# Performance work log

Measured on AMD Instinct MI355X. Metric: run time of the kernel, lower is better.

## Reference

```python
import jax, jax.numpy as jnp
import numpy as np

N = 50000        # num_nodes
E = 800000       # num_edges
D = 128          # hidden_dim == attention_dim
H = 4            # heads
DK = D // H      # d_k per head
STEP = 0.25      # args.step_size
NSTEPS = 4       # euler steps for t: 0 -> 1


def setup_inputs() -> dict:
    key = jax.random.key(0)
    k0, k1, k2, k3 = jax.random.split(key, 4)
    x = jax.random.normal(k0, (N, D), dtype=jnp.float32)
    edge_index = jax.random.randint(k1, (2, E), 0, N, dtype=jnp.int64)
    W_Q = jax.random.normal(k2, (D, D), dtype=jnp.float32) * 0.02
    b_Q = jnp.zeros((D,), jnp.float32)
    W_K = jax.random.normal(k3, (D, D), dtype=jnp.float32) * 0.02
    b_K = jnp.zeros((D,), jnp.float32)
    return {"x": x, "W_Q": W_Q, "b_Q": b_Q, "W_K": W_K, "b_K": b_K,
            "edge_index": edge_index}


def _segment_softmax(scores, seg, num_segments):
    # numerically-stable softmax over edges grouped by seg (dst node)
    m = jax.ops.segment_max(scores, seg, num_segments=num_segments)
    e = jnp.exp(scores - m[seg])
    s = jax.ops.segment_sum(e, seg, num_segments=num_segments)
    return e / (s[seg] + 1e-16)


def reference(x, W_Q, b_Q, W_K, b_K, edge_index):
    src, dst = edge_index[0], edge_index[1]
    # multi-head Q/K projections: [N, H, DK]
    q = (x @ W_Q + b_Q).reshape(N, H, DK)
    k = (x @ W_K + b_K).reshape(N, H, DK)
    # per-edge scaled-dot scores: [E, H]
    scores = jnp.sum(q[src] * k[dst], axis=-1) / np.sqrt(DK).astype(np.float32)
    # edge softmax normalized over edge[attention_norm_idx]=edge[1] (dst)
    att = _segment_softmax(scores, dst, N)          # [E, H]
    att_mean = jnp.mean(att, axis=1)                # [E] head-averaged, as in GRAND odefunc

    # fixed-step Euler integration of dx/dt = A x - x with A = attention spmm
    def euler_step(state, _):
        ax = jax.ops.segment_sum(att_mean[:, None] * state[dst], src,
                                 num_segments=N)    # ax[src] += att * x[dst]
        return state + STEP * (ax - state), None

    z, _ = jax.lax.scan(euler_step, x, None, length=NSTEPS)
    return z
```

## Files before the change

kernel.cpp:

```cpp
#include <hip/hip_runtime.h>
#include <hip/hip_fp16.h>

#define NODES 50000
#define EDGES 800000
#define HID   128
#define HEADS 4
#define SCORE_SCALE 0.17677669529663687f

#define NBUCK ((NODES + 255) >> 8)
#define CHUNK 4096

typedef unsigned int       u32;
typedef unsigned short     u16;
typedef unsigned long long u64;

typedef __attribute__((ext_vector_type(8))) short bf16x8;
typedef __attribute__((ext_vector_type(4))) float f32x4;

__device__ __forceinline__ u16 f2bf(float f) {
    u32 u = __builtin_bit_cast(u32, f);
    return (u16)((u + 0x7FFFu + ((u >> 16) & 1u)) >> 16);
}
__device__ __forceinline__ float bflo(u32 u) { return __builtin_bit_cast(float, u << 16); }
__device__ __forceinline__ float bfhi(u32 u) { return __builtin_bit_cast(float, u & 0xFFFF0000u); }
__device__ __forceinline__ float bdot2(u32 a, u32 b) {
    return bflo(a) * bflo(b) + bfhi(a) * bfhi(b);
}
__device__ __forceinline__ float2 h2f2(u32 u) {
    __half2 h = __builtin_bit_cast(__half2, u);
    return __half22float2(h);
}
__device__ __forceinline__ u32 f2h2(float a, float b) {
    __half2 h = __floats2half2_rn(a, b);
    return __builtin_bit_cast(u32, h);
}

__global__ __launch_bounds__(256) void wprep(
    const float* __restrict__ Wq, const float* __restrict__ Wk,
    u16* __restrict__ Wqt, u16* __restrict__ Wkt)
{
    int e   = blockIdx.x * 256 + threadIdx.x;
    int mat = e >> 14;
    int idx = e & 16383;
    int k  = idx >> 7;
    int nn = idx & 127;
    const float* W = mat ? Wk : Wq;
    u16*        Wt = mat ? Wkt : Wqt;
    Wt[nn * 128 + k] = f2bf(W[idx]);
}

__global__ __launch_bounds__(256) void gemm_qk_mfma(
    const float* __restrict__ x,
    const u16* __restrict__ Wqt, const float* __restrict__ bq,
    const u16* __restrict__ Wkt, const float* __restrict__ bk,
    u16* __restrict__ qb, u16* __restrict__ kb, u16* __restrict__ xh, int n)
{
    const int l  = threadIdx.x & 63;
    const int w  = threadIdx.x >> 6;
    const int lr = l & 15;
    const int kg = l >> 4;

    const int arow   = blockIdx.x * 64 + w * 16 + lr;
    const bool av    = (arow < n);
    const int  arowc = av ? arow : (n - 1);

    bf16x8 afrag[4];
    #pragma unroll
    for (int ks = 0; ks < 4; ++ks) {
        const float* px = x + (size_t)arowc * HID + ks * 32 + kg * 8;
        float4 p0 = *(const float4*)px;
        float4 p1 = *(const float4*)(px + 4);
        uint4 pk;
        pk.x = (u32)f2bf(p0.x) | ((u32)f2bf(p0.y) << 16);
        pk.y = (u32)f2bf(p0.z) | ((u32)f2bf(p0.w) << 16);
        pk.z = (u32)f2bf(p1.x) | ((u32)f2bf(p1.y) << 16);
        pk.w = (u32)f2bf(p1.z) | ((u32)f2bf(p1.w) << 16);
        afrag[ks] = __builtin_bit_cast(bf16x8, pk);
        if (av) {
            uint4 ph;
            ph.x = f2h2(p0.x, p0.y);
            ph.y = f2h2(p0.z, p0.w);
            ph.z = f2h2(p1.x, p1.y);
            ph.w = f2h2(p1.z, p1.w);
            *(uint4*)(xh + (size_t)arow * HID + ks * 32 + kg * 8) = ph;
        }
    }

    #pragma unroll
    for (int mat = 0; mat < 2; ++mat) {
        const u16*   Wt   = mat ? Wkt : Wqt;
        const float* bias = mat ? bk : bq;
        u16*         outp = mat ? kb : qb;

        #pragma unroll
        for (int cb = 0; cb < 8; ++cb) {
            float bc = bias[cb * 16 + lr];
            f32x4 acc = {bc, bc, bc, bc};
            #pragma unroll
            for (int ks = 0; ks < 4; ++ks) {
                bf16x8 bfrag = __builtin_bit_cast(bf16x8,
                    *(const uint4*)(Wt + (size_t)(cb * 16 + lr) * 128 + ks * 32 + kg * 8));
                acc = __builtin_amdgcn_mfma_f32_16x16x32_bf16(afrag[ks], bfrag, acc, 0, 0, 0);
            }
            #pragma unroll
            for (int reg = 0; reg < 4; ++reg) {
                int gr = blockIdx.x * 64 + w * 16 + kg * 4 + reg;
                if (gr < n) outp[(size_t)gr * HID + cb * 16 + lr] = f2bf(acc[reg]);
            }
        }
    }
}

__global__ __launch_bounds__(256) void hist_kernel(
    const int* __restrict__ ei, int* __restrict__ deg)
{
    int i = blockIdx.x * 256 + threadIdx.x;
    if (i < EDGES) atomicAdd(&deg[ei[i]], 1);
}

__global__ __launch_bounds__(1024) void scan1(
    const int* __restrict__ deg, int* __restrict__ off,
    int* __restrict__ part, int n)
{
    __shared__ int sd[1024];
    int t = threadIdx.x, i = blockIdx.x * 1024 + t;
    int v = (i < n) ? deg[i] : 0;
    sd[t] = v;
    __syncthreads();
    #pragma unroll
    for (int o = 1; o < 1024; o <<= 1) {
        int a = (t >= o) ? sd[t - o] : 0;
        __syncthreads();
        sd[t] += a;
        __syncthreads();
    }
    if (i < n) off[i] = sd[t] - v;
    if (t == 1023) part[blockIdx.x] = sd[1023];
}

__global__ __launch_bounds__(64) void scan2(int* __restrict__ part,
                                            int* __restrict__ off_n, int nb)
{
    int t = threadIdx.x;
    int v = (t < nb) ? part[t] : 0;
    int orig = v;
    #pragma unroll
    for (int o = 1; o < 64; o <<= 1) {
        int a = __shfl_up(v, o);
        if (t >= o) v += a;
    }
    if (t < nb) part[t] = v - orig;
    if (t == 63) *off_n = v;
}

__global__ __launch_bounds__(1024) void scan3(
    int* __restrict__ off, int* __restrict__ bcur,
    const int* __restrict__ part, int n)
{
    int i = blockIdx.x * 1024 + threadIdx.x;
    if (i < n) {
        int o = off[i] + part[blockIdx.x];
        off[i] = o;
        if ((i & 255) == 0) bcur[i >> 8] = o;
    }
}

__global__ __launch_bounds__(256) void bin_edges(
    const int* __restrict__ ei, int* __restrict__ bcur, u32* __restrict__ tmp)
{
    __shared__ u32 buf[CHUNK];
    __shared__ int hist[NBUCK];
    __shared__ int lcur[NBUCK];

    const int t  = threadIdx.x;
    const int e0 = blockIdx.x * CHUNK;
    const int e1 = (e0 + CHUNK < EDGES) ? e0 + CHUNK : EDGES;
    const int cnt = e1 - e0;

    for (int b = t; b < NBUCK; b += 256) hist[b] = 0;
    __syncthreads();

    for (int i = t; i < cnt; i += 256) {
        int src = ei[e0 + i];
        int dst = ei[EDGES + e0 + i];
        buf[i] = (u32)dst | ((u32)(src & 255) << 16) | ((u32)(src >> 8) << 24);
        atomicAdd(&hist[src >> 8], 1);
    }
    __syncthreads();

    for (int b = t; b < NBUCK; b += 256) {
        int h = hist[b];
        lcur[b] = h ? atomicAdd(&bcur[b], h) : 0;
    }
    __syncthreads();

    for (int i = t; i < cnt; i += 256) {
        u32 pk  = buf[i];
        int b   = pk >> 24;
        int pos = atomicAdd(&lcur[b], 1);
        tmp[pos] = pk & 0x00FFFFFFu;
    }
}

__global__ __launch_bounds__(256) void place_edges(
    const u32* __restrict__ tmp, const int* __restrict__ off,
    u32* __restrict__ epack, int n)
{
    __shared__ int lcur[256];
    const int t     = threadIdx.x;
    const int nbase = blockIdx.x << 8;
    const int nend  = (nbase + 256 < n) ? nbase + 256 : n;

    if (nbase + t < nend) lcur[t] = off[nbase + t];
    __syncthreads();

    const int s0 = off[nbase];
    const int s1 = off[nend];
    for (int i = s0 + t; i < s1; i += 256) {
        u32 pk    = tmp[i];
        int local = pk >> 16;
        int pos   = atomicAdd(&lcur[local], 1);
        epack[pos] = pk & 0xFFFFu;
    }
}

__global__ __launch_bounds__(256) void score_csr(
    const u16* __restrict__ qb, const u16* __restrict__ kb,
    const int* __restrict__ off, const u32* __restrict__ ccol,
    u16* __restrict__ evals16, float* __restrict__ nsum, int n)
{
    const int wv   = (blockIdx.x * 256 + threadIdx.x) >> 6;
    const int lane = threadIdx.x & 63;
    const int l16  = lane & 15;
    const int grp  = lane >> 4;
    if (wv >= n) return;

    const int beg = off[wv];
    const int end = off[wv + 1];

    uint4 qv = *(const uint4*)(qb + (size_t)wv * HID + l16 * 8);

    for (int j = beg; j < end; j += 16) {
        u32 d[4]; uint4 kv[4];
        #pragma unroll
        for (int u = 0; u < 4; ++u) {
            int e  = j + grp + u * 4;
            int ec = (e < end) ? e : (end - 1);
            d[u] = ccol[ec];
        }
        #pragma unroll
        for (int u = 0; u < 4; ++u)
            kv[u] = *(const uint4*)(kb + (size_t)d[u] * HID + l16 * 8);
        #pragma unroll
        for (int u = 0; u < 4; ++u) {
            int e = j + grp + u * 4;
            float p = bdot2(qv.x, kv[u].x) + bdot2(qv.y, kv[u].y) +
                      bdot2(qv.z, kv[u].z) + bdot2(qv.w, kv[u].w);
            p += __shfl_xor(p, 1);
            p += __shfl_xor(p, 2);
            if (e < end && (l16 & 3) == 0) {
                int head = l16 >> 2;
                float ev = __expf(p * SCORE_SCALE);
                evals16[(size_t)e * HEADS + head] = f2bf(ev);
                atomicAdd(&nsum[(size_t)d[u] * HEADS + head], ev);
            }
        }
    }
}

__global__ __launch_bounds__(256) void finalize_kernel(
    const u16* __restrict__ evals16, const float* __restrict__ nsum,
    u32* __restrict__ epack)
{
    int pos = blockIdx.x * 256 + threadIdx.x;
    if (pos >= EDGES) return;
    u32 dst = epack[pos];
    u64 ev8 = *(const u64*)(evals16 + (size_t)pos * HEADS);
    u32 lo = (u32)ev8, hi = (u32)(ev8 >> 32);
    float4 sv = *(const float4*)(nsum + (size_t)dst * HEADS);
    float am = 0.25f * (bflo(lo) / (sv.x + 1e-16f) + bfhi(lo) / (sv.y + 1e-16f) +
                        bflo(hi) / (sv.z + 1e-16f) + bfhi(hi) / (sv.w + 1e-16f));
    epack[pos] = dst | ((u32)f2bf(am) << 16);
}

template<int FINAL>
__global__ __launch_bounds__(256) void spmv_h(
    const u16* __restrict__ inh, u16* __restrict__ outh,
    float* __restrict__ outf,
    const int* __restrict__ off, const u32* __restrict__ epack, int n)
{
    const int w    = (blockIdx.x * 256 + threadIdx.x) >> 6;
    const int lane = threadIdx.x & 63;
    if (w >= n) return;

    const int beg = __builtin_amdgcn_readfirstlane(off[w]);
    const int end = __builtin_amdgcn_readfirstlane(off[w + 1]);

    const u32* inw = (const u32*)inh;

    float ax = 0.f, ay = 0.f;
    int j = beg;
    for (; j + 8 <= end; j += 8) {
        u32 e[8], s[8];
        #pragma unroll
        for (int u = 0; u < 8; ++u) e[u] = epack[j + u];
        #pragma unroll
        for (int u = 0; u < 8; ++u)
            s[u] = inw[(size_t)(e[u] & 0xFFFFu) * 64 + lane];
        #pragma unroll
        for (int u = 0; u < 8; ++u) {
            float vv = bfhi(e[u]);
            float2 sv = h2f2(s[u]);
            ax += vv * sv.x;
            ay += vv * sv.y;
        }
    }
    for (; j + 4 <= end; j += 4) {
        u32 e[4], s[4];
        #pragma unroll
        for (int u = 0; u < 4; ++u) e[u] = epack[j + u];
        #pragma unroll
        for (int u = 0; u < 4; ++u)
            s[u] = inw[(size_t)(e[u] & 0xFFFFu) * 64 + lane];
        #pragma unroll
        for (int u = 0; u < 4; ++u) {
            float vv = bfhi(e[u]);
            float2 sv = h2f2(s[u]);
            ax += vv * sv.x;
            ay += vv * sv.y;
        }
    }
    for (; j < end; ++j) {
        u32 e = epack[j];
        u32 s = inw[(size_t)(e & 0xFFFFu) * 64 + lane];
        float vv = bfhi(e);
        float2 sv = h2f2(s);
        ax += vv * sv.x;
        ay += vv * sv.y;
    }

    u32 zi = inw[(size_t)w * 64 + lane];
    float2 xi = h2f2(zi);
    const float ox = 0.75f * xi.x + 0.25f * ax;
    const float oy = 0.75f * xi.y + 0.25f * ay;
    if (FINAL) {
        float2 o; o.x = ox; o.y = oy;
        *(float2*)(outf + (size_t)w * HID + lane * 2) = o;
    } else {
        *(u32*)(outh + (size_t)w * HID + lane * 2) = f2h2(ox, oy);
    }
}

extern "C" void kernel_launch(void* const* d_in, const int* in_sizes, int n_in,
                              void* d_out, int out_size, void* d_ws, size_t ws_size,
                              hipStream_t stream)
{
    (void)in_sizes; (void)n_in; (void)out_size; (void)ws_size;

    const float* x  = (const float*)d_in[0];
    const float* Wq = (const float*)d_in[1];
    const float* bq = (const float*)d_in[2];
    const float* Wk = (const float*)d_in[3];
    const float* bk = (const float*)d_in[4];
    const int*   ei = (const int*)d_in[5];
    float* out = (float*)d_out;

    const int N = NODES, E = EDGES;
    const size_t ROWB_B = (size_t)N * HID * 2;

    char* ws = (char*)d_ws;
    u16*   qb    = (u16*)(ws);
    u16*   kb    = (u16*)(ws + ROWB_B);
    u16*   z1    = (u16*)(ws);
    u16*   z2    = (u16*)(ws + ROWB_B);
    ws += 2 * ROWB_B;
    u16*   xh    = (u16*)ws;  ws += ROWB_B;
    u16*   evals16 = (u16*)ws;
    u16*   z3    = (u16*)ws;  ws += (size_t)E * HEADS * 4;
    float* nsum  = (float*)ws; ws += (size_t)N * HEADS * 4;
    int*   deg   = (int*)ws;   ws += (size_t)N * 4;
    int*   off   = (int*)ws;   ws += ((size_t)(N + 1) * 4 + 255) & ~255ull;
    int*   bcur  = (int*)ws;   ws += ((size_t)NBUCK * 4 + 255) & ~255ull;
    int*   part  = (int*)ws;   ws += 256;
    u32*   epack = (u32*)ws;   ws += (size_t)E * 4;
    u32*   tmp   = (u32*)ws;   ws += (size_t)E * 4;
    u16*   Wqt   = (u16*)ws;   ws += (size_t)128 * 128 * 2;
    u16*   Wkt   = (u16*)ws;   ws += (size_t)128 * 128 * 2;

    hipMemsetAsync(nsum, 0, (size_t)N * HEADS * 4 + (size_t)N * 4, stream);

    wprep<<<128, 256, 0, stream>>>(Wq, Wk, Wqt, Wkt);

    gemm_qk_mfma<<<(N + 63) / 64, 256, 0, stream>>>(
        x, Wqt, bq, Wkt, bk, qb, kb, xh, N);

    hist_kernel<<<E / 256, 256, 0, stream>>>(ei, deg);

    const int nb = (N + 1023) / 1024;
    scan1<<<nb, 1024, 0, stream>>>(deg, off, part, N);
    scan2<<<1, 64, 0, stream>>>(part, off + N, nb);
    scan3<<<nb, 1024, 0, stream>>>(off, bcur, part, N);

    bin_edges<<<(E + CHUNK - 1) / CHUNK, 256, 0, stream>>>(ei, bcur, tmp);
    place_edges<<<NBUCK, 256, 0, stream>>>(tmp, off, epack, N);

    score_csr<<<(N * 64 + 255) / 256, 256, 0, stream>>>(
        qb, kb, off, epack, evals16, nsum, N);

    finalize_kernel<<<E / 256, 256, 0, stream>>>(evals16, nsum, epack);

    const int sg = (N * 64 + 255) / 256;
    spmv_h<0><<<sg, 256, 0, stream>>>(xh, z1, nullptr, off, epack, N);
    spmv_h<0><<<sg, 256, 0, stream>>>(z1, z2, nullptr, off, epack, N);
    spmv_h<0><<<sg, 256, 0, stream>>>(z2, z3, nullptr, off, epack, N);
    spmv_h<1><<<sg, 256, 0, stream>>>(z3, nullptr, out, off, epack, N);
}
```

Measured before the change: 286.5 us.

## Store K and gathered SpMV node features in FP8 to halve gather traffic

Stores the K projection and per-step node states in FP8 alongside the existing bf16/fp16 copies. The score kernel and the SpMV gathers now read 8-bit neighbour rows, while self terms still come from fp16. This halves the bytes moved by the random per-edge gathers, which dominate memory traffic. The cost is extra FP8 writes, a reworked workspace layout, and a large loss of precision in scores and aggregated features that could break accuracy tolerance.

```diff
diff --git a/kernel.cpp b/kernel.cpp
--- a/kernel.cpp
+++ b/kernel.cpp
@@ -12,10 +12,12 @@
 
 typedef unsigned int       u32;
 typedef unsigned short     u16;
+typedef unsigned char      u8;
 typedef unsigned long long u64;
 
 typedef __attribute__((ext_vector_type(8))) short bf16x8;
 typedef __attribute__((ext_vector_type(4))) float f32x4;
+typedef __attribute__((ext_vector_type(2))) float f32x2;
 
 __device__ __forceinline__ u16 f2bf(float f) {
     u32 u = __builtin_bit_cast(u32, f);
@@ -23,9 +25,6 @@
 }
 __device__ __forceinline__ float bflo(u32 u) { return __builtin_bit_cast(float, u << 16); }
 __device__ __forceinline__ float bfhi(u32 u) { return __builtin_bit_cast(float, u & 0xFFFF0000u); }
-__device__ __forceinline__ float bdot2(u32 a, u32 b) {
-    return bflo(a) * bflo(b) + bfhi(a) * bfhi(b);
-}
 __device__ __forceinline__ float2 h2f2(u32 u) {
     __half2 h = __builtin_bit_cast(__half2, u);
     return __half22float2(h);
@@ -53,7 +52,8 @@
     const float* __restrict__ x,
     const u16* __restrict__ Wqt, const float* __restrict__ bq,
     const u16* __restrict__ Wkt, const float* __restrict__ bk,
-    u16* __restrict__ qb, u16* __restrict__ kb, u16* __restrict__ xh, int n)
+    u16* __restrict__ qb, u8* __restrict__ k8,
+    u16* __restrict__ xh, u8* __restrict__ x8, int n)
 {
     const int l  = threadIdx.x & 63;
     const int w  = threadIdx.x >> 6;
@@ -83,6 +83,12 @@
             ph.z = f2h2(p1.x, p1.y);
             ph.w = f2h2(p1.z, p1.w);
             *(uint4*)(xh + (size_t)arow * HID + ks * 32 + kg * 8) = ph;
+            u32 w0 = __builtin_amdgcn_cvt_pk_fp8_f32(p0.x, p0.y, 0u, false);
+            w0     = __builtin_amdgcn_cvt_pk_fp8_f32(p0.z, p0.w, w0, true);
+            u32 w1 = __builtin_amdgcn_cvt_pk_fp8_f32(p1.x, p1.y, 0u, false);
+            w1     = __builtin_amdgcn_cvt_pk_fp8_f32(p1.z, p1.w, w1, true);
+            uint2 pv; pv.x = w0; pv.y = w1;
+            *(uint2*)(x8 + (size_t)arow * HID + ks * 32 + kg * 8) = pv;
         }
     }
 
@@ -90,7 +96,6 @@
     for (int mat = 0; mat < 2; ++mat) {
         const u16*   Wt   = mat ? Wkt : Wqt;
         const float* bias = mat ? bk : bq;
-        u16*         outp = mat ? kb : qb;
 
         #pragma unroll
         for (int cb = 0; cb < 8; ++cb) {
@@ -105,7 +110,14 @@
             #pragma unroll
             for (int reg = 0; reg < 4; ++reg) {
                 int gr = blockIdx.x * 64 + w * 16 + kg * 4 + reg;
-                if (gr < n) outp[(size_t)gr * HID + cb * 16 + lr] = f2bf(acc[reg]);
+                if (gr < n) {
+                    if (mat == 0) {
+                        qb[(size_t)gr * HID + cb * 16 + lr] = f2bf(acc[reg]);
+                    } else {
+                        u32 p8 = __builtin_amdgcn_cvt_pk_fp8_f32(acc[reg], 0.f, 0u, false);
+                        k8[(size_t)gr * HID + cb * 16 + lr] = (u8)(p8 & 0xFFu);
+                    }
+                }
             }
         }
     }
@@ -225,7 +237,7 @@
 }
 
 __global__ __launch_bounds__(256) void score_csr(
-    const u16* __restrict__ qb, const u16* __restrict__ kb,
+    const u16* __restrict__ qb, const u8* __restrict__ k8,
     const int* __restrict__ off, const u32* __restrict__ ccol,
     u16* __restrict__ evals16, float* __restrict__ nsum, int n)
 {
@@ -241,7 +253,7 @@
     uint4 qv = *(const uint4*)(qb + (size_t)wv * HID + l16 * 8);
 
     for (int j = beg; j < end; j += 16) {
-        u32 d[4]; uint4 kv[4];
+        u32 d[4]; u64 kv[4];
         #pragma unroll
         for (int u = 0; u < 4; ++u) {
             int e  = j + grp + u * 4;
@@ -250,12 +262,19 @@
         }
         #pragma unroll
         for (int u = 0; u < 4; ++u)
-            kv[u] = *(const uint4*)(kb + (size_t)d[u] * HID + l16 * 8);
+            kv[u] = *(const u64*)(k8 + (size_t)d[u] * HID + l16 * 8);
         #pragma unroll
         for (int u = 0; u < 4; ++u) {
             int e = j + grp + u * 4;
-            float p = bdot2(qv.x, kv[u].x) + bdot2(qv.y, kv[u].y) +
-                      bdot2(qv.z, kv[u].z) + bdot2(qv.w, kv[u].w);
+            u32 klo = (u32)kv[u], khi = (u32)(kv[u] >> 32);
+            f32x2 a = __builtin_amdgcn_cvt_pk_f32_fp8(klo, false);
+            f32x2 b = __builtin_amdgcn_cvt_pk_f32_fp8(klo, true);
+            f32x2 c = __builtin_amdgcn_cvt_pk_f32_fp8(khi, false);
+            f32x2 dd= __builtin_amdgcn_cvt_pk_f32_fp8(khi, true);
+            float p = bflo(qv.x) * a.x + bfhi(qv.x) * a.y
+                    + bflo(qv.y) * b.x + bfhi(qv.y) * b.y
+                    + bflo(qv.z) * c.x + bfhi(qv.z) * c.y
+                    + bflo(qv.w) * dd.x + bfhi(qv.w) * dd.y;
             p += __shfl_xor(p, 1);
             p += __shfl_xor(p, 2);
             if (e < end && (l16 & 3) == 0) {
@@ -284,8 +303,9 @@
 }
 
 template<int FINAL>
-__global__ __launch_bounds__(256) void spmv_h(
-    const u16* __restrict__ inh, u16* __restrict__ outh,
+__global__ __launch_bounds__(256) void spmv_h8(
+    const u16* __restrict__ inh, const u8* __restrict__ in8,
+    u16* __restrict__ outh, u8* __restrict__ out8,
     float* __restrict__ outf,
     const int* __restrict__ off, const u32* __restrict__ epack, int n)
 {
@@ -296,7 +316,7 @@
     const int beg = __builtin_amdgcn_readfirstlane(off[w]);
     const int end = __builtin_amdgcn_readfirstlane(off[w + 1]);
 
-    const u32* inw = (const u32*)inh;
+    const u16* in8w = (const u16*)in8;
 
     float ax = 0.f, ay = 0.f;
     int j = beg;
@@ -306,11 +326,11 @@
         for (int u = 0; u < 8; ++u) e[u] = epack[j + u];
         #pragma unroll
         for (int u = 0; u < 8; ++u)
-            s[u] = inw[(size_t)(e[u] & 0xFFFFu) * 64 + lane];
+            s[u] = in8w[(size_t)(e[u] & 0xFFFFu) * 64 + lane];
         #pragma unroll
         for (int u = 0; u < 8; ++u) {
             float vv = bfhi(e[u]);
-            float2 sv = h2f2(s[u]);
+            f32x2 sv = __builtin_amdgcn_cvt_pk_f32_fp8(s[u], false);
             ax += vv * sv.x;
             ay += vv * sv.y;
         }
@@ -321,25 +341,25 @@
         for (int u = 0; u < 4; ++u) e[u] = epack[j + u];
         #pragma unroll
         for (int u = 0; u < 4; ++u)
-            s[u] = inw[(size_t)(e[u] & 0xFFFFu) * 64 + lane];
+            s[u] = in8w[(size_t)(e[u] & 0xFFFFu) * 64 + lane];
         #pragma unroll
         for (int u = 0; u < 4; ++u) {
             float vv = bfhi(e[u]);
-            float2 sv = h2f2(s[u]);
+            f32x2 sv = __builtin_amdgcn_cvt_pk_f32_fp8(s[u], false);
             ax += vv * sv.x;
             ay += vv * sv.y;
         }
     }
     for (; j < end; ++j) {
         u32 e = epack[j];
-        u32 s = inw[(size_t)(e & 0xFFFFu) * 64 + lane];
+        u32 s = in8w[(size_t)(e & 0xFFFFu) * 64 + lane];
         float vv = bfhi(e);
-        float2 sv = h2f2(s);
+        f32x2 sv = __builtin_amdgcn_cvt_pk_f32_fp8(s, false);
         ax += vv * sv.x;
         ay += vv * sv.y;
     }
 
-    u32 zi = inw[(size_t)w * 64 + lane];
+    u32 zi = *(const u32*)(inh + (size_t)w * HID + lane * 2);
     float2 xi = h2f2(zi);
     const float ox = 0.75f * xi.x + 0.25f * ax;
     const float oy = 0.75f * xi.y + 0.25f * ay;
@@ -348,6 +368,8 @@
         *(float2*)(outf + (size_t)w * HID + lane * 2) = o;
     } else {
         *(u32*)(outh + (size_t)w * HID + lane * 2) = f2h2(ox, oy);
+        u32 p8 = __builtin_amdgcn_cvt_pk_fp8_f32(ox, oy, 0u, false);
+        ((u16*)out8)[(size_t)w * 64 + lane] = (u16)(p8 & 0xFFFFu);
     }
 }
 
@@ -366,33 +388,37 @@
     float* out = (float*)d_out;
 
     const int N = NODES, E = EDGES;
-    const size_t ROWB_B = (size_t)N * HID * 2;
+    const size_t ROWB_H = (size_t)N * HID * 2;
+    const size_t ROWB_8 = (size_t)N * HID;
 
     char* ws = (char*)d_ws;
-    u16*   qb    = (u16*)(ws);
-    u16*   kb    = (u16*)(ws + ROWB_B);
-    u16*   z1    = (u16*)(ws);
-    u16*   z2    = (u16*)(ws + ROWB_B);
-    ws += 2 * ROWB_B;
-    u16*   xh    = (u16*)ws;  ws += ROWB_B;
+    u16*   qb   = (u16*)ws;
+    u16*   z2h  = (u16*)ws;  ws += ROWB_H;
+    u8*    k8   = (u8*)ws;
+    u8*    z28  = (u8*)ws;   ws += ROWB_8;
+    u16*   xh   = (u16*)ws;
+    u16*   z3h  = (u16*)ws;  ws += ROWB_H;
+    u8*    x8   = (u8*)ws;
+    u8*    z38  = (u8*)ws;   ws += ROWB_8;
     u16*   evals16 = (u16*)ws;
-    u16*   z3    = (u16*)ws;  ws += (size_t)E * HEADS * 4;
-    float* nsum  = (float*)ws; ws += (size_t)N * HEADS * 4;
-    int*   deg   = (int*)ws;   ws += (size_t)N * 4;
-    int*   off   = (int*)ws;   ws += ((size_t)(N + 1) * 4 + 255) & ~255ull;
-    int*   bcur  = (int*)ws;   ws += ((size_t)NBUCK * 4 + 255) & ~255ull;
-    int*   part  = (int*)ws;   ws += 256;
-    u32*   epack = (u32*)ws;   ws += (size_t)E * 4;
-    u32*   tmp   = (u32*)ws;   ws += (size_t)E * 4;
-    u16*   Wqt   = (u16*)ws;   ws += (size_t)128 * 128 * 2;
-    u16*   Wkt   = (u16*)ws;   ws += (size_t)128 * 128 * 2;
+    u8*    z18  = (u8*)ws;   ws += (size_t)E * HEADS * 2;
+    u16*   z1h  = (u16*)ws;  ws += ROWB_H;
+    float* nsum = (float*)ws; ws += (size_t)N * HEADS * 4;
+    int*   deg  = (int*)ws;   ws += (size_t)N * 4;
+    int*   off  = (int*)ws;   ws += ((size_t)(N + 1) * 4 + 255) & ~255ull;
+    int*   bcur = (int*)ws;   ws += ((size_t)NBUCK * 4 + 255) & ~255ull;
+    int*   part = (int*)ws;   ws += 256;
+    u32*   epack = (u32*)ws;  ws += (size_t)E * 4;
+    u32*   tmp   = (u32*)ws;  ws += (size_t)E * 4;
+    u16*   Wqt   = (u16*)ws;  ws += (size_t)128 * 128 * 2;
+    u16*   Wkt   = (u16*)ws;  ws += (size_t)128 * 128 * 2;
 
     hipMemsetAsync(nsum, 0, (size_t)N * HEADS * 4 + (size_t)N * 4, stream);
 
     wprep<<<128, 256, 0, stream>>>(Wq, Wk, Wqt, Wkt);
 
     gemm_qk_mfma<<<(N + 63) / 64, 256, 0, stream>>>(
-        x, Wqt, bq, Wkt, bk, qb, kb, xh, N);
+        x, Wqt, bq, Wkt, bk, qb, k8, xh, x8, N);
 
     hist_kernel<<<E / 256, 256, 0, stream>>>(ei, deg);
 
@@ -405,13 +431,13 @@
     place_edges<<<NBUCK, 256, 0, stream>>>(tmp, off, epack, N);
 
     score_csr<<<(N * 64 + 255) / 256, 256, 0, stream>>>(
-        qb, kb, off, epack, evals16, nsum, N);
+        qb, k8, off, epack, evals16, nsum, N);
 
     finalize_kernel<<<E / 256, 256, 0, stream>>>(evals16, nsum, epack);
 
     const int sg = (N * 64 + 255) / 256;
-    spmv_h<0><<<sg, 256, 0, stream>>>(xh, z1, nullptr, off, epack, N);
-    spmv_h<0><<<sg, 256, 0, stream>>>(z1, z2, nullptr, off, epack, N);
-    spmv_h<0><<<sg, 256, 0, stream>>>(z2, z3, nullptr, off, epack, N);
-    spmv_h<1><<<sg, 256, 0, stream>>>(z3, nullptr, out, off, epack, N);
-}
+    spmv_h8<0><<<sg, 256, 0, stream>>>(xh,  x8,  z1h, z18, nullptr, off, epack, N);
+    spmv_h8<0><<<sg, 256, 0, stream>>>(z1h, z18, z2h, z28, nullptr, off, epack, N);
+    spmv_h8<0><<<sg, 256, 0, stream>>>(z2h, z28, z3h, z38, nullptr, off, epack, N);
+    spmv_h8<1><<<sg, 256, 0, stream>>>(z3h, z38, nullptr, nullptr, out, off, epack, N);
+}
```

New measurement: 265.5 us. -7.3%, faster.
